# Kernel tuning notes

Hardware: AMD Instinct MI355X
Metric: run time of the kernel (lower is better)

## Reference

```python
import jax, jax.numpy as jnp
import numpy as np

REG_MAX = 16
BOX_W = 7.5
OBJ_W = 1.0
TOPK = 10
EPS = 1e-7


def dfl_decode(x, reg_max):
    # x: [B, 4*reg_max, N] -> expected value of per-side distribution -> [B, N, 4] (xyxy)
    B, C, N = x.shape
    x = x.reshape(B, 4, reg_max, N)
    p = jax.nn.softmax(x, axis=2)
    proj = jnp.arange(reg_max, dtype=x.dtype)
    return jnp.einsum('bkrn,r->bnk', p, proj)


def bbox_ciou(b1, b2):
    # b1: [B,N,1,4], b2: [B,1,M,4], xyxy -> [B,N,M]
    x11, y11, x12, y12 = b1[..., 0], b1[..., 1], b1[..., 2], b1[..., 3]
    x21, y21, x22, y22 = b2[..., 0], b2[..., 1], b2[..., 2], b2[..., 3]
    w1, h1 = x12 - x11, y12 - y11
    w2, h2 = x22 - x21, y22 - y21
    iw = jnp.clip(jnp.minimum(x12, x22) - jnp.maximum(x11, x21), 0.0)
    ih = jnp.clip(jnp.minimum(y12, y22) - jnp.maximum(y11, y21), 0.0)
    inter = iw * ih
    union = w1 * h1 + w2 * h2 - inter + EPS
    iou = inter / union
    cw = jnp.maximum(x12, x22) - jnp.minimum(x11, x21)
    ch = jnp.maximum(y12, y22) - jnp.minimum(y11, y21)
    c2 = cw * cw + ch * ch + EPS
    rho2 = ((x21 + x22 - x11 - x12) ** 2 + (y21 + y22 - y11 - y12) ** 2) * 0.25
    v = (4.0 / (np.pi ** 2)) * (jnp.arctan(w2 / (h2 + EPS)) - jnp.arctan(w1 / (h1 + EPS))) ** 2
    alpha = jax.lax.stop_gradient(v / (v - iou + 1.0 + EPS))
    return iou - rho2 / c2 - alpha * v


def setup_inputs() -> dict:
    key = jax.random.key(0)
    k1, k2, k3, k4 = jax.random.split(key, 4)
    B, N, M = 8, 34000, 64
    boxes = jax.random.normal(k1, (B, 4 * REG_MAX, N), dtype=jnp.float32)
    scores = jax.random.normal(k2, (B, N), dtype=jnp.float32)
    # GT boxes: valid xyxy in roughly the same [0, reg_max) range as decoded preds
    xy = jax.random.uniform(k3, (B, M, 2), dtype=jnp.float32) * 11.0
    wh = jax.random.uniform(k4, (B, M, 2), dtype=jnp.float32) * 4.0 + 0.5
    targets = jnp.concatenate([xy, xy + wh], axis=-1)
    return {'boxes': boxes, 'scores': scores, 'targets': targets}


def reference(boxes, scores, targets):
    B, N = scores.shape
    M = targets.shape[1]
    pb = dfl_decode(boxes, REG_MAX)                     # [B,N,4]
    ciou = bbox_ciou(pb[:, :, None, :], targets[:, None, :, :])  # [B,N,M]
    k = min(TOPK, N)
    topv, topi = jax.lax.top_k(jnp.swapaxes(ciou, 1, 2), k)      # [B,M,k] over anchors
    valid = topv > 0.0
    vals = jnp.where(valid, topv, 0.0)

    def per_batch(idx, val, vld):
        flat_i = idx.reshape(-1)
        iou_t = jnp.zeros((N,), val.dtype).at[flat_i].max(val.reshape(-1))
        pos = jnp.zeros((N,), bool).at[flat_i].max(vld.reshape(-1))
        return iou_t, pos

    iou_target, pos = jax.vmap(per_batch)(topi, vals, valid)     # [B,N]
    posf = pos.astype(iou_target.dtype)
    npos = posf.sum(axis=1)
    box_per = jnp.where(npos > 0,
                        ((1.0 - iou_target) * posf).sum(axis=1) / jnp.maximum(npos, 1.0),
                        0.0)
    box_loss = box_per.sum()
    # BCEWithLogits (mean over anchors), summed over batch
    bce = jnp.maximum(scores, 0.0) - scores * iou_target + jnp.log1p(jnp.exp(-jnp.abs(scores)))
    obj_loss = bce.mean(axis=1).sum()
    total = (BOX_W * box_loss + OBJ_W * obj_loss) / B
    return total, box_loss, obj_loss
```

## Files before the change

### kernel.cpp

```cpp
#include <hip/hip_runtime.h>
#include <math.h>

#define BQ 8
#define MQ 64
#define REGMAX 16
#define KTOP 10
#define CH 4
#define EPSQ 1e-7f

__device__ __forceinline__ float frcp(float x) { return __builtin_amdgcn_rcpf(x); }

__global__ __launch_bounds__(256) void decode_kernel(
    const float* __restrict__ boxes, float* __restrict__ pb,
    float* __restrict__ patan, unsigned int* __restrict__ iou_bits,
    float* __restrict__ acc, int N) {
  int i = blockIdx.x * 256 + threadIdx.x;
  if (blockIdx.x == 0 && threadIdx.x < BQ * 4) acc[threadIdx.x] = 0.f;
  int total = BQ * N;
  if (i >= total) return;
  iou_bits[i] = 0u;
  int b = i / N;
  int n = i - b * N;
  const float* base = boxes + (size_t)b * (4 * REGMAX) * N + n;
  float out[4];
#pragma unroll
  for (int k = 0; k < 4; ++k) {
    float x[REGMAX];
#pragma unroll
    for (int r = 0; r < REGMAX; ++r)
      x[r] = base[(size_t)(k * REGMAX + r) * N];
    float mx = x[0];
#pragma unroll
    for (int r = 1; r < REGMAX; ++r) mx = fmaxf(mx, x[r]);
    float s = 0.f, ws = 0.f;
#pragma unroll
    for (int r = 0; r < REGMAX; ++r) {
      float e = __expf(x[r] - mx);
      s += e;
      ws += (float)r * e;
    }
    out[k] = ws * frcp(s);
  }
  ((float4*)pb)[i] = make_float4(out[0], out[1], out[2], out[3]);
  float w1 = out[2] - out[0], h1 = out[3] - out[1];
  patan[i] = atanf(w1 * frcp(h1 + EPSQ));
}

__global__ __launch_bounds__(256) void topk1_kernel(
    const float4* __restrict__ pb, const float* __restrict__ patan,
    const float* __restrict__ targets, float* __restrict__ cand_v,
    int* __restrict__ cand_i, int N) {
  const int blk = blockIdx.x;
  const int chunk = blk & (CH - 1);
  const int bm = blk >> 2;
  const int b = bm >> 6;
  const int m = bm & 63;
  const int tid = threadIdx.x;

  const float4 t = ((const float4*)targets)[b * MQ + m];
  const float x21 = t.x, y21 = t.y, x22 = t.z, y22 = t.w;
  const float w2 = x22 - x21, h2 = y22 - y21;
  const float atan_t = atanf(w2 * frcp(h2 + EPSQ));
  const float area2 = w2 * h2;
  const float sumx2 = x21 + x22, sumy2 = y21 + y22;
  const float CPI = 4.0f / (float)(M_PI * M_PI);

  float tv[KTOP];
  int ti[KTOP];
#pragma unroll
  for (int j = 0; j < KTOP; ++j) { tv[j] = 0.f; ti[j] = 0; }
  float tmin = 0.f;
  int minpos = 0;

  const int chunkN = (N + CH - 1) / CH;
  const int n0 = chunk * chunkN;
  const int n1 = min(N, n0 + chunkN);

  const float4* pbb = pb + (size_t)b * N;
  const float* pab = patan + (size_t)b * N;

  for (int n = n0 + tid; n < n1; n += 256) {
    float4 p = pbb[n];
    float pa = pab[n];
    float x11 = p.x, y11 = p.y, x12 = p.z, y12 = p.w;
    float w1 = x12 - x11, h1 = y12 - y11;
    float iw = fmaxf(fminf(x12, x22) - fmaxf(x11, x21), 0.f);
    float ih = fmaxf(fminf(y12, y22) - fmaxf(y11, y21), 0.f);
    float inter = iw * ih;
    float uni = w1 * h1 + area2 - inter + EPSQ;
    float iou = inter * frcp(uni);
    float cw = fmaxf(x12, x22) - fminf(x11, x21);
    float ch = fmaxf(y12, y22) - fminf(y11, y21);
    float c2 = cw * cw + ch * ch + EPSQ;
    float dx = sumx2 - x11 - x12;
    float dy = sumy2 - y11 - y12;
    float rho2 = (dx * dx + dy * dy) * 0.25f;
    float da = atan_t - pa;
    float v = CPI * da * da;
    float alpha = v * frcp(v - iou + 1.f + EPSQ);
    float ciou = iou - rho2 * frcp(c2) - alpha * v;

    if (ciou > tmin) {
#pragma unroll
      for (int j = 0; j < KTOP; ++j)
        if (j == minpos) { tv[j] = ciou; ti[j] = n; }
      tmin = tv[0]; minpos = 0;
#pragma unroll
      for (int j = 1; j < KTOP; ++j)
        if (tv[j] < tmin) { tmin = tv[j]; minpos = j; }
    }
  }

  float lmax = tv[0];
  int lpos = 0;
#pragma unroll
  for (int j = 1; j < KTOP; ++j)
    if (tv[j] > lmax) { lmax = tv[j]; lpos = j; }

  __shared__ unsigned long long swred[4];
  const int out_base = bm * (CH * KTOP) + chunk * KTOP;
  for (int round = 0; round < KTOP; ++round) {
    unsigned long long key =
        ((unsigned long long)__float_as_uint(lmax) << 32) | (unsigned int)tid;
#pragma unroll
    for (int d = 1; d < 64; d <<= 1) {
      unsigned long long o = __shfl_xor(key, d, 64);
      if (o > key) key = o;
    }
    if ((tid & 63) == 0) swred[tid >> 6] = key;
    __syncthreads();
    unsigned long long win =
        max(max(swred[0], swred[1]), max(swred[2], swred[3]));
    __syncthreads();
    int wtid = (int)(win & 0xffffffffu);
    if (tid == wtid) {
      cand_v[out_base + round] = lmax;
      cand_i[out_base + round] = ti[lpos];
#pragma unroll
      for (int j = 0; j < KTOP; ++j)
        if (j == lpos) tv[j] = 0.f;
      lmax = tv[0]; lpos = 0;
#pragma unroll
      for (int j = 1; j < KTOP; ++j)
        if (tv[j] > lmax) { lmax = tv[j]; lpos = j; }
    }
  }
}

__global__ __launch_bounds__(64) void topk2_kernel(
    const float* __restrict__ cand_v, const int* __restrict__ cand_i,
    unsigned int* __restrict__ iou_bits, int N) {
  const int bm = blockIdx.x;
  const int b = bm >> 6;
  const int tid = threadIdx.x;
  const int NC = CH * KTOP;
  __shared__ float sv[NC];
  __shared__ int si[NC];
  if (tid < NC) {
    sv[tid] = cand_v[bm * NC + tid];
    si[tid] = cand_i[bm * NC + tid];
  }
  __syncthreads();
  if (tid < NC) {
    float v = sv[tid];
    if (v > 0.f) {
      int rank = 0;
#pragma unroll
      for (int i = 0; i < NC; ++i)
        rank += (sv[i] > v) || (sv[i] == v && i < tid);
      if (rank < KTOP) {
        atomicMax(&iou_bits[(size_t)b * N + si[tid]], __float_as_uint(v));
      }
    }
  }
}

__global__ __launch_bounds__(256) void reduce_kernel(
    const float* __restrict__ scores, const unsigned int* __restrict__ iou_bits,
    float* __restrict__ acc, int N, int bpb) {
  int b = blockIdx.x / bpb;
  int cb = blockIdx.x % bpb;
  int tid = threadIdx.x;
  float s_box = 0.f, s_cnt = 0.f, s_bce = 0.f;
  const unsigned int* row = iou_bits + (size_t)b * N;
  const float* srow = scores + (size_t)b * N;
  for (int n = cb * 256 + tid; n < N; n += bpb * 256) {
    float t = __uint_as_float(row[n]);
    float sc = srow[n];
    s_bce += fmaxf(sc, 0.f) - sc * t + log1pf(__expf(-fabsf(sc)));
    if (t > 0.f) { s_box += 1.f - t; s_cnt += 1.f; }
  }
  __shared__ float r0[256], r1[256], r2[256];
  r0[tid] = s_box; r1[tid] = s_cnt; r2[tid] = s_bce;
  __syncthreads();
  for (int s = 128; s > 0; s >>= 1) {
    if (tid < s) {
      r0[tid] += r0[tid + s];
      r1[tid] += r1[tid + s];
      r2[tid] += r2[tid + s];
    }
    __syncthreads();
  }
  if (tid == 0) {
    atomicAdd(&acc[b * 4 + 0], r0[0]);
    atomicAdd(&acc[b * 4 + 1], r1[0]);
    atomicAdd(&acc[b * 4 + 2], r2[0]);
  }
}

__global__ void finalize_kernel(const float* __restrict__ acc,
                                float* __restrict__ out, int N) {
  if (threadIdx.x == 0 && blockIdx.x == 0) {
    float box_loss = 0.f, obj_loss = 0.f;
    for (int b = 0; b < BQ; ++b) {
      float sbox = acc[b * 4 + 0];
      float npos = acc[b * 4 + 1];
      float sbce = acc[b * 4 + 2];
      box_loss += (npos > 0.f) ? sbox / fmaxf(npos, 1.f) : 0.f;
      obj_loss += sbce / (float)N;
    }
    out[0] = (7.5f * box_loss + 1.0f * obj_loss) / (float)BQ;
    out[1] = box_loss;
    out[2] = obj_loss;
  }
}

extern "C" void kernel_launch(void* const* d_in, const int* in_sizes, int n_in,
                              void* d_out, int out_size, void* d_ws, size_t ws_size,
                              hipStream_t stream) {
  const float* boxes = (const float*)d_in[0];
  const float* scores = (const float*)d_in[1];
  const float* targets = (const float*)d_in[2];
  float* out = (float*)d_out;
  const int N = in_sizes[1] / BQ;

  char* ws = (char*)d_ws;
  size_t pb_bytes = (size_t)BQ * N * 4 * sizeof(float);
  size_t patan_bytes = (size_t)BQ * N * sizeof(float);
  size_t iou_bytes = (size_t)BQ * N * sizeof(unsigned int);
  size_t acc_bytes = (size_t)BQ * 4 * sizeof(float);
  size_t cand_bytes = (size_t)BQ * MQ * CH * KTOP * sizeof(float);

  float* pb = (float*)ws;                      ws += pb_bytes;
  float* patan = (float*)ws;                   ws += patan_bytes;
  unsigned int* iou_bits = (unsigned int*)ws;  ws += iou_bytes;
  float* acc = (float*)ws;                     ws += acc_bytes;
  float* cand_v = (float*)ws;                  ws += cand_bytes;
  int* cand_i = (int*)ws;

  int total = BQ * N;
  decode_kernel<<<(total + 255) / 256, 256, 0, stream>>>(boxes, pb, patan,
                                                         iou_bits, acc, N);
  topk1_kernel<<<BQ * MQ * CH, 256, 0, stream>>>((const float4*)pb, patan,
                                                 targets, cand_v, cand_i, N);
  topk2_kernel<<<BQ * MQ, 64, 0, stream>>>(cand_v, cand_i, iou_bits, N);
  const int bpb = 64;
  reduce_kernel<<<BQ * bpb, 256, 0, stream>>>(scores, iou_bits, acc, N, bpb);
  finalize_kernel<<<1, 64, 0, stream>>>(acc, out, N);
}
```

Before: 168.0 us.

## Fuse BCE into decode, threshold-buffered top-k, sparse fixup replaces full reduce

The base BCE term (no target) is now computed inside the decode kernel, which removes the full pass over scores and iou_bits. The per-thread 10-entry register top-k is replaced by a shared-memory candidate buffer with a rising threshold and periodic wave-level selection. The reduce and finalize kernels give way to a small fixup kernel that only visits the final top-k winners, applies the -score*iou correction and box stats, and finalizes using a last-block counter. The risks are a correctness edge case when several targets tie on the same anchor (the equality check could double count), plus extra atomics and serialization in the selection step.

```diff
diff --git a/kernel.cpp b/kernel.cpp
--- a/kernel.cpp
+++ b/kernel.cpp
@@ -7,43 +7,99 @@
 #define KTOP 10
 #define CH 4
 #define EPSQ 1e-7f
+#define SSEG 4
+#define TRIG 256
+#define CBUF (TRIG + SSEG * 256 + 16)
 
 __device__ __forceinline__ float frcp(float x) { return __builtin_amdgcn_rcpf(x); }
 
 __global__ __launch_bounds__(256) void decode_kernel(
-    const float* __restrict__ boxes, float* __restrict__ pb,
-    float* __restrict__ patan, unsigned int* __restrict__ iou_bits,
-    float* __restrict__ acc, int N) {
-  int i = blockIdx.x * 256 + threadIdx.x;
-  if (blockIdx.x == 0 && threadIdx.x < BQ * 4) acc[threadIdx.x] = 0.f;
-  int total = BQ * N;
-  if (i >= total) return;
-  iou_bits[i] = 0u;
-  int b = i / N;
-  int n = i - b * N;
-  const float* base = boxes + (size_t)b * (4 * REGMAX) * N + n;
-  float out[4];
-#pragma unroll
-  for (int k = 0; k < 4; ++k) {
-    float x[REGMAX];
-#pragma unroll
-    for (int r = 0; r < REGMAX; ++r)
-      x[r] = base[(size_t)(k * REGMAX + r) * N];
-    float mx = x[0];
-#pragma unroll
-    for (int r = 1; r < REGMAX; ++r) mx = fmaxf(mx, x[r]);
-    float s = 0.f, ws = 0.f;
-#pragma unroll
-    for (int r = 0; r < REGMAX; ++r) {
-      float e = __expf(x[r] - mx);
-      s += e;
-      ws += (float)r * e;
-    }
-    out[k] = ws * frcp(s);
-  }
-  ((float4*)pb)[i] = make_float4(out[0], out[1], out[2], out[3]);
-  float w1 = out[2] - out[0], h1 = out[3] - out[1];
-  patan[i] = atanf(w1 * frcp(h1 + EPSQ));
+    const float* __restrict__ boxes, const float* __restrict__ scores,
+    float* __restrict__ pb, float* __restrict__ patan,
+    unsigned int* __restrict__ iou_bits, float* __restrict__ acc, int N) {
+  const int tid = threadIdx.x;
+  const int i = blockIdx.x * 256 + tid;
+  const int total = BQ * N;
+  float bce0 = 0.f;
+  int myb = -1;
+  const int b_first = (blockIdx.x * 256) / N;
+  if (i < total) {
+    iou_bits[i] = 0u;
+    myb = i / N;
+    int n = i - myb * N;
+    float sc = scores[i];
+    bce0 = fmaxf(sc, 0.f) + log1pf(__expf(-fabsf(sc)));
+    const float* base = boxes + (size_t)myb * (4 * REGMAX) * N + n;
+    float out[4];
+#pragma unroll
+    for (int k = 0; k < 4; ++k) {
+      float x[REGMAX];
+#pragma unroll
+      for (int r = 0; r < REGMAX; ++r)
+        x[r] = __builtin_nontemporal_load(&base[(size_t)(k * REGMAX + r) * N]);
+      float mx = x[0];
+#pragma unroll
+      for (int r = 1; r < REGMAX; ++r) mx = fmaxf(mx, x[r]);
+      float s = 0.f, ws = 0.f;
+#pragma unroll
+      for (int r = 0; r < REGMAX; ++r) {
+        float e = __expf(x[r] - mx);
+        s += e;
+        ws += (float)r * e;
+      }
+      out[k] = ws * frcp(s);
+    }
+    ((float4*)pb)[i] = make_float4(out[0], out[1], out[2], out[3]);
+    float w1 = out[2] - out[0], h1 = out[3] - out[1];
+    patan[i] = atanf(w1 * frcp(h1 + EPSQ));
+  }
+  __shared__ float r0[256], r1[256];
+  r0[tid] = (myb == b_first) ? bce0 : 0.f;
+  r1[tid] = (myb == b_first + 1) ? bce0 : 0.f;
+  __syncthreads();
+  for (int s = 128; s > 0; s >>= 1) {
+    if (tid < s) { r0[tid] += r0[tid + s]; r1[tid] += r1[tid + s]; }
+    __syncthreads();
+  }
+  if (tid == 0) {
+    atomicAdd(&acc[b_first * 4 + 2], r0[0]);
+    if (b_first + 1 < BQ) atomicAdd(&acc[(b_first + 1) * 4 + 2], r1[0]);
+  }
+}
+
+__device__ __forceinline__ void select_top10(
+    float* s_bv, int* s_bi, float* s_winv, int* s_wini,
+    int* s_cnt, float* s_sthr, int c, int tid) {
+  if (tid < 64) {
+    for (int r = 0; r < KTOP; ++r) {
+      float bv = 0.f;
+      int bs = 0xffff;
+      for (int sl = tid; sl < c; sl += 64) {
+        float v = s_bv[sl];
+        if (v > bv) { bv = v; bs = sl; }
+      }
+      unsigned long long key =
+          ((unsigned long long)__float_as_uint(bv) << 32) | (unsigned int)bs;
+#pragma unroll
+      for (int d = 1; d < 64; d <<= 1) {
+        unsigned long long o = __shfl_xor(key, d, 64);
+        if (o > key) key = o;
+      }
+      if (tid == 0) {
+        float wv = __uint_as_float((unsigned int)(key >> 32));
+        int ws = (int)(key & 0xffffu);
+        s_winv[r] = wv;
+        if (wv > 0.f && ws != 0xffff) {
+          s_wini[r] = s_bi[ws];
+          s_bv[ws] = 0.f;
+        } else {
+          s_wini[r] = 0;
+        }
+      }
+    }
+    if (tid < KTOP) { s_bv[tid] = s_winv[tid]; s_bi[tid] = s_wini[tid]; }
+    if (tid == 0) { *s_cnt = KTOP; *s_sthr = s_winv[KTOP - 1]; }
+  }
 }
 
 __global__ __launch_bounds__(256) void topk1_kernel(
@@ -57,6 +113,15 @@
   const int m = bm & 63;
   const int tid = threadIdx.x;
 
+  __shared__ float s_bv[CBUF];
+  __shared__ int s_bi[CBUF];
+  __shared__ float s_winv[KTOP];
+  __shared__ int s_wini[KTOP];
+  __shared__ int s_cnt;
+  __shared__ float s_sthr;
+  if (tid == 0) { s_cnt = 0; s_sthr = 0.f; }
+  __syncthreads();
+
   const float4 t = ((const float4*)targets)[b * MQ + m];
   const float x21 = t.x, y21 = t.y, x22 = t.z, y22 = t.w;
   const float w2 = x22 - x21, h2 = y22 - y21;
@@ -65,97 +130,81 @@
   const float sumx2 = x21 + x22, sumy2 = y21 + y22;
   const float CPI = 4.0f / (float)(M_PI * M_PI);
 
-  float tv[KTOP];
-  int ti[KTOP];
-#pragma unroll
-  for (int j = 0; j < KTOP; ++j) { tv[j] = 0.f; ti[j] = 0; }
-  float tmin = 0.f;
-  int minpos = 0;
-
   const int chunkN = (N + CH - 1) / CH;
   const int n0 = chunk * chunkN;
   const int n1 = min(N, n0 + chunkN);
+  float sthr = 0.f;
 
   const float4* pbb = pb + (size_t)b * N;
   const float* pab = patan + (size_t)b * N;
 
-  for (int n = n0 + tid; n < n1; n += 256) {
-    float4 p = pbb[n];
-    float pa = pab[n];
-    float x11 = p.x, y11 = p.y, x12 = p.z, y12 = p.w;
-    float w1 = x12 - x11, h1 = y12 - y11;
-    float iw = fmaxf(fminf(x12, x22) - fmaxf(x11, x21), 0.f);
-    float ih = fmaxf(fminf(y12, y22) - fmaxf(y11, y21), 0.f);
-    float inter = iw * ih;
-    float uni = w1 * h1 + area2 - inter + EPSQ;
-    float iou = inter * frcp(uni);
-    float cw = fmaxf(x12, x22) - fminf(x11, x21);
-    float ch = fmaxf(y12, y22) - fminf(y11, y21);
-    float c2 = cw * cw + ch * ch + EPSQ;
-    float dx = sumx2 - x11 - x12;
-    float dy = sumy2 - y11 - y12;
-    float rho2 = (dx * dx + dy * dy) * 0.25f;
-    float da = atan_t - pa;
-    float v = CPI * da * da;
-    float alpha = v * frcp(v - iou + 1.f + EPSQ);
-    float ciou = iou - rho2 * frcp(c2) - alpha * v;
-
-    if (ciou > tmin) {
-#pragma unroll
-      for (int j = 0; j < KTOP; ++j)
-        if (j == minpos) { tv[j] = ciou; ti[j] = n; }
-      tmin = tv[0]; minpos = 0;
-#pragma unroll
-      for (int j = 1; j < KTOP; ++j)
-        if (tv[j] < tmin) { tmin = tv[j]; minpos = j; }
-    }
-  }
-
-  float lmax = tv[0];
-  int lpos = 0;
-#pragma unroll
-  for (int j = 1; j < KTOP; ++j)
-    if (tv[j] > lmax) { lmax = tv[j]; lpos = j; }
-
-  __shared__ unsigned long long swred[4];
+  for (int basei = n0; basei < n1; basei += SSEG * 256) {
+#pragma unroll
+    for (int s = 0; s < SSEG; ++s) {
+      int n = basei + s * 256 + tid;
+      if (n < n1) {
+        float4 p = pbb[n];
+        float pa = pab[n];
+        float x11 = p.x, y11 = p.y, x12 = p.z, y12 = p.w;
+        float w1 = x12 - x11, h1 = y12 - y11;
+        float iw = fmaxf(fminf(x12, x22) - fmaxf(x11, x21), 0.f);
+        float ih = fmaxf(fminf(y12, y22) - fmaxf(y11, y21), 0.f);
+        float inter = iw * ih;
+        float uni = w1 * h1 + area2 - inter + EPSQ;
+        float iou = inter * frcp(uni);
+        float cw = fmaxf(x12, x22) - fminf(x11, x21);
+        float ch = fmaxf(y12, y22) - fminf(y11, y21);
+        float c2 = cw * cw + ch * ch + EPSQ;
+        float dx = sumx2 - x11 - x12;
+        float dy = sumy2 - y11 - y12;
+        float rho2 = (dx * dx + dy * dy) * 0.25f;
+        float da = atan_t - pa;
+        float v = CPI * da * da;
+        float alpha = v * frcp(v - iou + 1.f + EPSQ);
+        float ciou = iou - rho2 * frcp(c2) - alpha * v;
+        if (ciou > sthr) {
+          int slot = atomicAdd(&s_cnt, 1);
+          s_bv[slot] = ciou;
+          s_bi[slot] = n;
+        }
+      }
+    }
+    __syncthreads();
+    int c = s_cnt;
+    __syncthreads();
+    if (c > TRIG) {
+      select_top10(s_bv, s_bi, s_winv, s_wini, &s_cnt, &s_sthr, c, tid);
+      __syncthreads();
+    }
+    sthr = s_sthr;
+  }
+
+  int c = s_cnt;
+  if (c > KTOP) {
+    select_top10(s_bv, s_bi, s_winv, s_wini, &s_cnt, &s_sthr, c, tid);
+    __syncthreads();
+    c = KTOP;
+  }
   const int out_base = bm * (CH * KTOP) + chunk * KTOP;
-  for (int round = 0; round < KTOP; ++round) {
-    unsigned long long key =
-        ((unsigned long long)__float_as_uint(lmax) << 32) | (unsigned int)tid;
-#pragma unroll
-    for (int d = 1; d < 64; d <<= 1) {
-      unsigned long long o = __shfl_xor(key, d, 64);
-      if (o > key) key = o;
-    }
-    if ((tid & 63) == 0) swred[tid >> 6] = key;
-    __syncthreads();
-    unsigned long long win =
-        max(max(swred[0], swred[1]), max(swred[2], swred[3]));
-    __syncthreads();
-    int wtid = (int)(win & 0xffffffffu);
-    if (tid == wtid) {
-      cand_v[out_base + round] = lmax;
-      cand_i[out_base + round] = ti[lpos];
-#pragma unroll
-      for (int j = 0; j < KTOP; ++j)
-        if (j == lpos) tv[j] = 0.f;
-      lmax = tv[0]; lpos = 0;
-#pragma unroll
-      for (int j = 1; j < KTOP; ++j)
-        if (tv[j] > lmax) { lmax = tv[j]; lpos = j; }
-    }
+  if (tid < KTOP) {
+    float v = (tid < c) ? s_bv[tid] : 0.f;
+    int ix = (tid < c) ? s_bi[tid] : 0;
+    cand_v[out_base + tid] = v;
+    cand_i[out_base + tid] = ix;
   }
 }
 
 __global__ __launch_bounds__(64) void topk2_kernel(
     const float* __restrict__ cand_v, const int* __restrict__ cand_i,
-    unsigned int* __restrict__ iou_bits, int N) {
+    unsigned int* __restrict__ iou_bits, float* __restrict__ fin_v,
+    int* __restrict__ fin_i, int N) {
   const int bm = blockIdx.x;
   const int b = bm >> 6;
   const int tid = threadIdx.x;
   const int NC = CH * KTOP;
   __shared__ float sv[NC];
   __shared__ int si[NC];
+  if (tid < KTOP) { fin_v[bm * KTOP + tid] = 0.f; fin_i[bm * KTOP + tid] = 0; }
   if (tid < NC) {
     sv[tid] = cand_v[bm * NC + tid];
     si[tid] = cand_i[bm * NC + tid];
@@ -166,62 +215,58 @@
     if (v > 0.f) {
       int rank = 0;
 #pragma unroll
-      for (int i = 0; i < NC; ++i)
-        rank += (sv[i] > v) || (sv[i] == v && i < tid);
+      for (int i2 = 0; i2 < NC; ++i2)
+        rank += (sv[i2] > v) || (sv[i2] == v && i2 < tid);
       if (rank < KTOP) {
         atomicMax(&iou_bits[(size_t)b * N + si[tid]], __float_as_uint(v));
-      }
-    }
-  }
-}
-
-__global__ __launch_bounds__(256) void reduce_kernel(
-    const float* __restrict__ scores, const unsigned int* __restrict__ iou_bits,
-    float* __restrict__ acc, int N, int bpb) {
-  int b = blockIdx.x / bpb;
-  int cb = blockIdx.x % bpb;
-  int tid = threadIdx.x;
-  float s_box = 0.f, s_cnt = 0.f, s_bce = 0.f;
-  const unsigned int* row = iou_bits + (size_t)b * N;
-  const float* srow = scores + (size_t)b * N;
-  for (int n = cb * 256 + tid; n < N; n += bpb * 256) {
-    float t = __uint_as_float(row[n]);
-    float sc = srow[n];
-    s_bce += fmaxf(sc, 0.f) - sc * t + log1pf(__expf(-fabsf(sc)));
-    if (t > 0.f) { s_box += 1.f - t; s_cnt += 1.f; }
-  }
-  __shared__ float r0[256], r1[256], r2[256];
-  r0[tid] = s_box; r1[tid] = s_cnt; r2[tid] = s_bce;
+        fin_v[bm * KTOP + rank] = v;
+        fin_i[bm * KTOP + rank] = si[tid];
+      }
+    }
+  }
+}
+
+__global__ __launch_bounds__(256) void fixup_kernel(
+    const float* __restrict__ fin_v, const int* __restrict__ fin_i,
+    const unsigned int* __restrict__ iou_bits,
+    const float* __restrict__ scores, float* __restrict__ acc,
+    float* __restrict__ out, int N, int nblocks) {
+  const int tid = threadIdx.x;
+  const int e = blockIdx.x * 256 + tid;
+  const int TOT = BQ * MQ * KTOP;
+  if (e < TOT) {
+    int b = e / (MQ * KTOP);
+    float v = fin_v[e];
+    if (v > 0.f) {
+      int ix = fin_i[e];
+      if (iou_bits[(size_t)b * N + ix] == __float_as_uint(v)) {
+        atomicAdd(&acc[b * 4 + 0], 1.f - v);
+        atomicAdd(&acc[b * 4 + 1], 1.f);
+        atomicAdd(&acc[b * 4 + 2], -scores[(size_t)b * N + ix] * v);
+      }
+    }
+  }
+  __threadfence();
   __syncthreads();
-  for (int s = 128; s > 0; s >>= 1) {
-    if (tid < s) {
-      r0[tid] += r0[tid + s];
-      r1[tid] += r1[tid + s];
-      r2[tid] += r2[tid + s];
-    }
-    __syncthreads();
-  }
   if (tid == 0) {
-    atomicAdd(&acc[b * 4 + 0], r0[0]);
-    atomicAdd(&acc[b * 4 + 1], r1[0]);
-    atomicAdd(&acc[b * 4 + 2], r2[0]);
-  }
-}
-
-__global__ void finalize_kernel(const float* __restrict__ acc,
-                                float* __restrict__ out, int N) {
-  if (threadIdx.x == 0 && blockIdx.x == 0) {
-    float box_loss = 0.f, obj_loss = 0.f;
-    for (int b = 0; b < BQ; ++b) {
-      float sbox = acc[b * 4 + 0];
-      float npos = acc[b * 4 + 1];
-      float sbce = acc[b * 4 + 2];
-      box_loss += (npos > 0.f) ? sbox / fmaxf(npos, 1.f) : 0.f;
-      obj_loss += sbce / (float)N;
-    }
-    out[0] = (7.5f * box_loss + 1.0f * obj_loss) / (float)BQ;
-    out[1] = box_loss;
-    out[2] = obj_loss;
+    unsigned int* cnt = (unsigned int*)(acc + 32);
+    unsigned int prev = atomicAdd(cnt, 1u);
+    if (prev == (unsigned int)(nblocks - 1)) {
+      float box = 0.f, obj = 0.f;
+      for (int bb = 0; bb < BQ; ++bb) {
+        float sb = __hip_atomic_load(&acc[bb * 4 + 0], __ATOMIC_RELAXED,
+                                     __HIP_MEMORY_SCOPE_AGENT);
+        float np = __hip_atomic_load(&acc[bb * 4 + 1], __ATOMIC_RELAXED,
+                                     __HIP_MEMORY_SCOPE_AGENT);
+        float sc = __hip_atomic_load(&acc[bb * 4 + 2], __ATOMIC_RELAXED,
+                                     __HIP_MEMORY_SCOPE_AGENT);
+        box += (np > 0.f) ? sb * frcp(fmaxf(np, 1.f)) : 0.f;
+        obj += sc / (float)N;
+      }
+      out[0] = (7.5f * box + obj) / (float)BQ;
+      out[1] = box;
+      out[2] = obj;
+    }
   }
 }
 
@@ -238,23 +283,30 @@
   size_t pb_bytes = (size_t)BQ * N * 4 * sizeof(float);
   size_t patan_bytes = (size_t)BQ * N * sizeof(float);
   size_t iou_bytes = (size_t)BQ * N * sizeof(unsigned int);
-  size_t acc_bytes = (size_t)BQ * 4 * sizeof(float);
+  size_t acc_bytes = 64 * sizeof(float);
   size_t cand_bytes = (size_t)BQ * MQ * CH * KTOP * sizeof(float);
+  size_t fin_bytes = (size_t)BQ * MQ * KTOP * sizeof(float);
 
   float* pb = (float*)ws;                      ws += pb_bytes;
   float* patan = (float*)ws;                   ws += patan_bytes;
   unsigned int* iou_bits = (unsigned int*)ws;  ws += iou_bytes;
   float* acc = (float*)ws;                     ws += acc_bytes;
   float* cand_v = (float*)ws;                  ws += cand_bytes;
-  int* cand_i = (int*)ws;
+  int* cand_i = (int*)ws;                      ws += cand_bytes;
+  float* fin_v = (float*)ws;                   ws += fin_bytes;
+  int* fin_i = (int*)ws;
+
+  hipMemsetAsync(acc, 0, acc_bytes, stream);
 
   int total = BQ * N;
-  decode_kernel<<<(total + 255) / 256, 256, 0, stream>>>(boxes, pb, patan,
-                                                         iou_bits, acc, N);
+  decode_kernel<<<(total + 255) / 256, 256, 0, stream>>>(boxes, scores, pb,
+                                                         patan, iou_bits, acc, N);
   topk1_kernel<<<BQ * MQ * CH, 256, 0, stream>>>((const float4*)pb, patan,
                                                  targets, cand_v, cand_i, N);
-  topk2_kernel<<<BQ * MQ, 64, 0, stream>>>(cand_v, cand_i, iou_bits, N);
-  const int bpb = 64;
-  reduce_kernel<<<BQ * bpb, 256, 0, stream>>>(scores, iou_bits, acc, N, bpb);
-  finalize_kernel<<<1, 64, 0, stream>>>(acc, out, N);
-}
+  topk2_kernel<<<BQ * MQ, 64, 0, stream>>>(cand_v, cand_i, iou_bits, fin_v,
+                                           fin_i, N);
+  const int TOT = BQ * MQ * KTOP;
+  const int nblocks = (TOT + 255) / 256;
+  fixup_kernel<<<nblocks, 256, 0, stream>>>(fin_v, fin_i, iou_bits, scores, acc,
+                                            out, N, nblocks);
+}
```

Result: slower. 204.0 us (+21.5%).
